# Optimization experiments

Hardware: AMD Instinct MI355X
Metric: run time of the kernel (lower is better)

## Reference

```python
import jax, jax.numpy as jnp
import numpy as np

# ---- fixed configuration (see shape_source) ----
B, ND, NPR = 64, 32, 32          # batch, drug-subgraph nodes, protein-subgraph nodes
LD, LP = 100, 1000               # drug_MAX_LENGH, protein_MAX_LENGH
DIM, CONV = 64, 40               # char_dim, conv
DK, PK = (4, 6, 8), (4, 8, 12)   # drug_kernel, protein_kernel
VD, VP = 71, 26                  # SMILES / FASTA vocab sizes
ED, EP, EDP = 128, 128, 64       # DDI / PPI / DPI edges per subgraph
GNN_LAYERS = 2
SLOPE = 0.01                     # LeakyReLU default slope


def setup_inputs():
    key = jax.random.key(0)
    ks = iter(jax.random.split(key, 64))
    def nrm(shape, s=0.02):
        return jax.random.normal(next(ks), shape, jnp.float32) * s
    inp = {}
    inp['drug_tokens'] = jax.random.randint(next(ks), (B, LD), 0, VD, jnp.int32)
    inp['protein_tokens'] = jax.random.randint(next(ks), (B, LP), 0, VP, jnp.int32)
    inp['drug_node_tokens'] = jax.random.randint(next(ks), (B, ND, LD), 0, VD, jnp.int32)
    inp['protein_node_tokens'] = jax.random.randint(next(ks), (B, NPR, LP), 0, VP, jnp.int32)
    inp['ddi_edges'] = jax.random.randint(next(ks), (B, 2, ED), 0, ND, jnp.int32)
    inp['ppi_edges'] = jax.random.randint(next(ks), (B, 2, EP), 0, NPR, jnp.int32)
    inp['dpi_edges'] = jax.random.randint(next(ks), (B, 2, EDP), 0, min(ND, NPR), jnp.int32)
    # sequence embeddings (padding_idx=0 -> zero row)
    inp['drug_embed'] = nrm((VD, DIM)).at[0].set(0.)
    inp['protein_embed'] = nrm((VP, DIM)).at[0].set(0.)
    # drug CNN stack
    inp['dW1'], inp['db1'] = nrm((CONV, DIM, DK[0])), jnp.zeros((CONV,), jnp.float32)
    inp['dW2'], inp['db2'] = nrm((2*CONV, CONV, DK[1])), jnp.zeros((2*CONV,), jnp.float32)
    inp['dW3'], inp['db3'] = nrm((4*CONV, 2*CONV, DK[2])), jnp.zeros((4*CONV,), jnp.float32)
    # protein CNN stack
    inp['pW1'], inp['pb1'] = nrm((CONV, DIM, PK[0])), jnp.zeros((CONV,), jnp.float32)
    inp['pW2'], inp['pb2'] = nrm((2*CONV, CONV, PK[1])), jnp.zeros((2*CONV,), jnp.float32)
    inp['pW3'], inp['pb3'] = nrm((4*CONV, 2*CONV, PK[2])), jnp.zeros((4*CONV,), jnp.float32)
    # graph node-feature embedding tables (creat_drug_node / creat_protein_node)
    inp['drug_node_table'] = nrm((VD, LD)).at[0].set(0.)
    inp['protein_node_table'] = nrm((VP, LP)).at[0].set(0.)
    # SAGEConv params: Wl (neighbor path, has bias), Wr (root path, no bias)
    inp['ddi_Wl'], inp['ddi_bl'], inp['ddi_Wr'] = nrm((LD, LD)), jnp.zeros((LD,), jnp.float32), nrm((LD, LD))
    inp['ppi_Wl'], inp['ppi_bl'], inp['ppi_Wr'] = nrm((LP, LP)), jnp.zeros((LP,), jnp.float32), nrm((LP, LP))
    inp['dpi_Wl'], inp['dpi_bl'], inp['dpi_Wr'] = nrm((LP, LD)), jnp.zeros((LP,), jnp.float32), nrm((LP, LP))
    inp['pdi_Wl'], inp['pdi_bl'], inp['pdi_Wr'] = nrm((LD, LP)), jnp.zeros((LD,), jnp.float32), nrm((LD, LD))
    # fusion MLP
    inp['fc1_W'], inp['fc1_b'] = nrm((1024, 1420)), jnp.zeros((1024,), jnp.float32)
    inp['fc2_W'], inp['fc2_b'] = nrm((1024, 1024)), jnp.zeros((1024,), jnp.float32)
    inp['fc3_W'], inp['fc3_b'] = nrm((512, 1024)), jnp.zeros((512,), jnp.float32)
    inp['out_W'], inp['out_b'] = nrm((2, 512)), jnp.zeros((2,), jnp.float32)
    return inp


def _conv_relu(x, w, b):
    # x: [B, Cin, L], w: [Cout, Cin, K] -> valid Conv1d + ReLU
    y = jax.lax.conv_general_dilated(x, w, (1,), 'VALID',
                                     dimension_numbers=('NCH', 'OIH', 'NCH'))
    return jax.nn.relu(y + b[None, :, None])


def _node_feat(tokens, table, vocab):
    # mean over sequence of embedded tokens == (token-count histogram / L) @ table
    counts = jax.nn.one_hot(tokens, vocab, dtype=table.dtype).sum(axis=2)  # [B, N, V]
    return jnp.einsum('bnv,vd->bnd', counts, table) / tokens.shape[-1]


def _sage(xs, xd, edges, Wl, bl, Wr):
    # PyG SAGEConv, aggr='mean': lin_l(mean_j x_src[j]) + lin_r(x_dst)
    src, dst = edges[0], edges[1]
    n = xd.shape[0]
    s = jax.ops.segment_sum(xs[src], dst, num_segments=n)
    c = jax.ops.segment_sum(jnp.ones((src.shape[0],), xs.dtype), dst, num_segments=n)
    agg = s / jnp.maximum(c, 1.0)[:, None]
    return agg @ Wl.T + bl + xd @ Wr.T


def _forward(drug_tokens, protein_tokens, drug_node_tokens, protein_node_tokens,
             ddi_edges, ppi_edges, dpi_edges,
             drug_embed, protein_embed,
             dW1, db1, dW2, db2, dW3, db3,
             pW1, pb1, pW2, pb2, pW3, pb3,
             drug_node_table, protein_node_table,
             ddi_Wl, ddi_bl, ddi_Wr, ppi_Wl, ppi_bl, ppi_Wr,
             dpi_Wl, dpi_bl, dpi_Wr, pdi_Wl, pdi_bl, pdi_Wr,
             fc1_W, fc1_b, fc2_W, fc2_b, fc3_W, fc3_b, out_W, out_b):
    # --- CNN branches (maxpool kernel spans whole remaining length == global max) ---
    x = drug_embed[drug_tokens].transpose(0, 2, 1)            # [B, DIM, LD]
    for w, b in ((dW1, db1), (dW2, db2), (dW3, db3)):
        x = _conv_relu(x, w, b)
    drug_feat = x.max(axis=2)                                 # [B, 4*CONV]
    y = protein_embed[protein_tokens].transpose(0, 2, 1)      # [B, DIM, LP]
    for w, b in ((pW1, pb1), (pW2, pb2), (pW3, pb3)):
        y = _conv_relu(y, w, b)
    prot_feat = y.max(axis=2)                                 # [B, 4*CONV]
    # --- graph node features: mean over sequence of node-token embeddings ---
    dx = _node_feat(drug_node_tokens, drug_node_table, VD)    # [B, ND, LD]
    px = _node_feat(protein_node_tokens, protein_node_table, VP)  # [B, NPR, LP]
    # --- hetero SAGE message passing, aggr='mean' across relations ---
    def _hetero(dxi, pxi, ddi, ppi, dpi):
        pdi = dpi[::-1]
        d = 0.5 * (_sage(dxi, dxi, ddi, ddi_Wl, ddi_bl, ddi_Wr)
                   + _sage(pxi, dxi, pdi, pdi_Wl, pdi_bl, pdi_Wr))
        p = 0.5 * (_sage(pxi, pxi, ppi, ppi_Wl, ppi_bl, ppi_Wr)
                   + _sage(dxi, pxi, dpi, dpi_Wl, dpi_bl, dpi_Wr))
        return d, p
    hetero_b = jax.vmap(_hetero)
    for _ in range(GNN_LAYERS):
        dx, px = hetero_b(dx, px, ddi_edges, ppi_edges, dpi_edges)
    # node 0 of each subgraph is the query drug / protein
    graph_feat = jnp.concatenate([dx[:, 0], px[:, 0]], axis=-1)   # [B, LD+LP]
    # --- fusion MLP (dropout = identity at eval) ---
    pair = jnp.concatenate([drug_feat, prot_feat, graph_feat], axis=-1)  # [B, 1420]
    h = jax.nn.leaky_relu(pair @ fc1_W.T + fc1_b, SLOPE)
    h = jax.nn.leaky_relu(h @ fc2_W.T + fc2_b, SLOPE)
    h = jax.nn.leaky_relu(h @ fc3_W.T + fc3_b, SLOPE)
    return h @ out_W.T + out_b                                 # [B, 2]


def reference(drug_tokens, protein_tokens, drug_node_tokens, protein_node_tokens,
              ddi_edges, ppi_edges, dpi_edges,
              drug_embed, protein_embed,
              dW1, db1, dW2, db2, dW3, db3,
              pW1, pb1, pW2, pb2, pW3, pb3,
              drug_node_table, protein_node_table,
              ddi_Wl, ddi_bl, ddi_Wr, ppi_Wl, ppi_bl, ppi_Wr,
              dpi_Wl, dpi_bl, dpi_Wr, pdi_Wl, pdi_bl, pdi_Wr,
              fc1_W, fc1_b, fc2_W, fc2_b, fc3_W, fc3_b, out_W, out_b):
    return _forward(drug_tokens, protein_tokens, drug_node_tokens, protein_node_tokens,
                    ddi_edges, ppi_edges, dpi_edges,
                    drug_embed, protein_embed,
                    dW1, db1, dW2, db2, dW3, db3,
                    pW1, pb1, pW2, pb2, pW3, pb3,
                    drug_node_table, protein_node_table,
                    ddi_Wl, ddi_bl, ddi_Wr, ppi_Wl, ppi_bl, ppi_Wr,
                    dpi_Wl, dpi_bl, dpi_Wr, pdi_Wl, pdi_bl, pdi_Wr,
                    fc1_W, fc1_b, fc2_W, fc2_b, fc3_W, fc3_b, out_W, out_b)
```

## Files before the change

### kernel.cpp

```cpp
#include <hip/hip_runtime.h>
#include <hip/hip_bf16.h>


typedef __attribute__((ext_vector_type(8))) short short8;
typedef __attribute__((ext_vector_type(4))) float f32x4;
union FragU { uint32_t u[4]; uint4 q; short8 s; };

static __device__ inline unsigned short f2bf(float v) {
    __hip_bfloat16 h = __float2bfloat16(v);
    return *(unsigned short*)&h;
}

static constexpr size_t O_PAIR = 0;
static constexpr size_t O_CF1  = 363520;
static constexpr size_t O_CF2  = 625664;
static constexpr size_t O_CF3  = 887808;
static constexpr size_t Z1_END = 1018880;
static constexpr size_t O_H1   = 1018880;
static constexpr size_t O_H2   = 1281024;
static constexpr size_t O_H3   = 1543168;
static constexpr size_t O_BD   = 1674240;
static constexpr size_t O_BP   = 1674752;
static constexpr size_t O_WDS  = 1678848;
static constexpr size_t O_WPS  = 1998336;
static constexpr size_t O_WTP1 = 6520320;
static constexpr size_t O_WTP2 = 6585856;
static constexpr size_t O_WTP3 = 6667776;
static constexpr size_t O_WTD1 = 7159296;
static constexpr size_t O_WTD2 = 7224832;
static constexpr size_t O_WTD3 = 7306752;
static constexpr size_t AR     = 7552512;
static constexpr size_t A_AD  = AR + 0;
static constexpr size_t A_AP  = AR + 479232;
static constexpr size_t A_A2D = AR + 1327104;
static constexpr size_t A_A2P = AR + 1486848;
static constexpr size_t A_UD  = AR + 1769472;
static constexpr size_t A_UP  = AR + 1855488;
static constexpr size_t A_RHO = AR + 2641920;
static constexpr size_t Z2_CNT = 2641920 / 4;
static constexpr size_t A_Y2P = AR + 0;
static constexpr size_t A_Y1P = AR + 10158080;
static constexpr size_t A_Y1D = AR + 15278080;
static constexpr size_t A_Y2D = AR + 10158080;
static constexpr size_t NEED_BYTES = AR + 15810560;

__global__ void zero32_k(uint32_t* __restrict__ p, int n) {
    int i = blockIdx.x * 256 + threadIdx.x;
    if (i < n) p[i] = 0u;
}

__global__ void zero2_k(uint32_t* __restrict__ p1, int n1,
                        uint32_t* __restrict__ p2, int n2) {
    int i = blockIdx.x * 256 + threadIdx.x;
    if (i < n1) p1[i] = 0u;
    else if (i - n1 < n2) p2[i - n1] = 0u;
}

static constexpr long P0 = 100;
static constexpr long P1 = P0 + 1000;
static constexpr long P2 = P1 + 14336;
static constexpr long P3 = P2 + 14336;
static constexpr long P4 = P3 + 131072;
static constexpr long P5 = P4 + 1048576;
static constexpr long P6 = P5 + 1048576;
static constexpr long P7 = P6 + 163840;
static constexpr long P8 = P7 + 131072;
static constexpr long P9 = P8 + 32768;
static constexpr long P10 = P9 + 40960;
static constexpr long P11 = P10 + 245760;
static constexpr long P12 = P11 + 32768;
static constexpr long P13 = P12 + 40960;
static constexpr long P14 = P13 + 122880;
static constexpr long P15 = P14 + 70400;

__device__ inline void wt_block(unsigned short* dst, int ld_dst, int coloff,
                                const float* s1, const float* s2, int ld_src,
                                int N, int Kreal, int Kblk, long local) {
    int n = (int)(local / Kblk), k = (int)(local % Kblk);
    float v = 0.f;
    if (n < N && k < Kreal) {
        v = s1[(size_t)n * ld_src + k];
        if (s2) v += s2[(size_t)n * ld_src + k];
    }
    dst[(size_t)n * ld_dst + coloff + k] = f2bf(v);
}

__device__ inline void wtconv_block(unsigned short* dst, const float* W,
                                    int Co, int Ci, int K, int KP, long local) {
    int co = (int)(local / (Ci * KP));
    int rem = (int)(local % (Ci * KP));
    int ci = rem / KP, k = rem % KP;
    float v = (co < Co && k < K) ? W[((size_t)co * Ci + ci) * K + k] : 0.f;
    dst[local] = f2bf(v);
}

__global__ __launch_bounds__(256) void prep_k(
    float* bd, float* bp, unsigned short* WdS, unsigned short* WpS,
    unsigned short* WtP1, unsigned short* WtP2, unsigned short* WtP3,
    unsigned short* WtD1, unsigned short* WtD2, unsigned short* WtD3,
    float* pair,
    const float* ddi_Wl, const float* ddi_bl, const float* ddi_Wr,
    const float* ppi_Wl, const float* ppi_bl, const float* ppi_Wr,
    const float* dpi_Wl, const float* dpi_bl, const float* dpi_Wr,
    const float* pdi_Wl, const float* pdi_bl, const float* pdi_Wr,
    const float* dW1, const float* dW2, const float* dW3,
    const float* pW1, const float* pW2, const float* pW3) {
    long idx = (long)blockIdx.x * 256 + threadIdx.x;
    if (idx < P0) { bd[idx] = 0.5f * (ddi_bl[idx] + pdi_bl[idx]); return; }
    if (idx < P1) { long j = idx - P0; bp[j] = 0.5f * (ppi_bl[j] + dpi_bl[j]); return; }
    if (idx < P2) { wt_block(WdS, 1248, 0, ddi_Wl, nullptr, 100, 100, 100, 112, idx - P1); return; }
    if (idx < P3) { wt_block(WdS, 1248, 112, ddi_Wr, pdi_Wr, 100, 100, 100, 112, idx - P2); return; }
    if (idx < P4) { wt_block(WdS, 1248, 224, pdi_Wl, nullptr, 1000, 100, 1000, 1024, idx - P3); return; }
    if (idx < P5) { wt_block(WpS, 2208, 0, ppi_Wl, nullptr, 1000, 1000, 1000, 1024, idx - P4); return; }
    if (idx < P6) { wt_block(WpS, 2208, 1024, ppi_Wr, dpi_Wr, 1000, 1000, 1000, 1024, idx - P5); return; }
    if (idx < P7) { wt_block(WpS, 2208, 2048, dpi_Wl, nullptr, 100, 1000, 100, 160, idx - P6); return; }
    if (idx < P8)  { return; }
    if (idx < P9)  { wtconv_block(WtP1, pW1, 40, 64, 4, 8, idx - P8); return; }
    if (idx < P10) { wtconv_block(WtP2, pW2, 80, 40, 8, 8, idx - P9); return; }
    if (idx < P11) { wtconv_block(WtP3, pW3, 160, 80, 12, 16, idx - P10); return; }
    if (idx < P12) { wtconv_block(WtD1, dW1, 40, 64, 4, 8, idx - P11); return; }
    if (idx < P13) { wtconv_block(WtD2, dW2, 80, 40, 6, 8, idx - P12); return; }
    if (idx < P14) { wtconv_block(WtD3, dW3, 160, 80, 8, 8, idx - P13); return; }
    if (idx < P15) {
        long l = idx - P14;
        int b = (int)(l / 1100), j = (int)(l % 1100);
        if (j < 100) pair[(size_t)b * 1420 + 320 + j] = bd[j];
        else pair[(size_t)b * 1420 + 420 + (j - 100)] = bp[j - 100];
        return;
    }
}

__global__ __launch_bounds__(256) void gnn_front_k(const int* __restrict__ ddi,
                                                   const int* __restrict__ ppi,
                                                   const int* __restrict__ dpi,
                                                   const int* __restrict__ dtoks,
                                                   const int* __restrict__ ptoks,
                                                   const float* __restrict__ dtable,
                                                   const float* __restrict__ ptable,
                                                   float* __restrict__ RHO,
                                                   unsigned short* __restrict__ Ad,
                                                   unsigned short* __restrict__ Ap) {
    const int role = blockIdx.x, b = blockIdx.y, tid = threadIdx.x;
    __shared__ float M[4][32][32];
    __shared__ int cnt4[4][32];
// ... 107 lines not shown
                #pragma unroll
                for (int i = 0; i < 7; ++i) acc[i] += WC[i][v] * tv;
            }
            unsigned short h;
            h = f2bf(acc[0]); Ad[g0d + 224 + d] = h;
            h = f2bf(acc[1]); Ad[g1d_ + 224 + d] = h; Ap[g0p + 1024 + d] = h;
            h = f2bf(acc[2]); Ap[g0p + d] = h;
            h = f2bf(acc[3]); Ap[g1p + d] = h;
            h = f2bf(acc[4]); Ap[g1p + 1024 + d] = h; Ap[g2p + d] = h;
            h = f2bf(acc[5]); Ap[g2p + 1024 + d] = h;
            h = f2bf(acc[6]); Ad[g2d + 224 + d] = h;
        }
    }
}

__global__ __launch_bounds__(256) void gemm_sk3(const unsigned short* __restrict__ A, int lda,
                                                const unsigned short* __restrict__ Bm, int ldb,
                                                int K, int KS, float scale,
                                                float* __restrict__ out,
                                                int rs, int coloff, int Nw) {
    const int tid = threadIdx.x;
    const int lane = tid & 63, w = tid >> 6, c = lane & 15, q = lane >> 4;
    const int n = blockIdx.x * 64 + w * 16 + c;
    const int gz = blockIdx.z;
    const unsigned short* Ab = A + (size_t)gz * 64 * lda;
    const int Ks = ((K / KS + 31) / 32) * 32;
    const int k0 = blockIdx.y * Ks;
    const int k1 = min(K, k0 + Ks);
    f32x4 acc[4];
    #pragma unroll
    for (int i = 0; i < 4; ++i) acc[i] = (f32x4){0.f, 0.f, 0.f, 0.f};
    for (int k = k0; k < k1; k += 32) {
        FragU bf;
        bf.q = *(const uint4*)&Bm[(size_t)n * ldb + k + q * 8];
        #pragma unroll
        for (int i = 0; i < 4; ++i) {
            FragU af;
            af.q = *(const uint4*)&Ab[(size_t)(i * 16 + c) * lda + k + q * 8];
            acc[i] = __builtin_amdgcn_mfma_f32_16x16x32_bf16(af.s, bf.s, acc[i], 0, 0, 0);
        }
    }
    if (n >= Nw) return;
    #pragma unroll
    for (int i = 0; i < 4; ++i)
        #pragma unroll
        for (int r = 0; r < 4; ++r) {
            int m = gz * 64 + i * 16 + q * 4 + r;
            atomicAdd(&out[(size_t)m * rs + coloff + n], scale * acc[i][r]);
        }
}

__global__ void ep_k(const float* __restrict__ Ud, const float* __restrict__ Up,
                     const float* __restrict__ RHO,
                     const float* __restrict__ bd, const float* __restrict__ bp,
                     unsigned short* __restrict__ A2d, unsigned short* __restrict__ A2p) {
    int idx = blockIdx.x * 256 + threadIdx.x;
    if (idx < 192 * 112) {
        int m = idx / 112, n = idx % 112;
        if (n >= 100) return;
        int g = m >> 6, b = m & 63;
        float rho = (g == 0) ? RHO[b * 4 + 0] : (g == 1) ? 1.f : RHO[b * 4 + 3];
        unsigned short h = f2bf(Ud[idx] + rho * bd[n]);
        if (g == 0) A2d[(size_t)b * 1248 + n] = h;
        else if (g == 1) A2d[(size_t)b * 1248 + 112 + n] = h;
        else A2p[(size_t)b * 2208 + 2048 + n] = h;
    } else {
        int l = idx - 192 * 112;
        if (l >= 192 * 1024) return;
        int m = l / 1024, n = l % 1024;
        if (n >= 1000) return;
        int g = m >> 6, b = m & 63;
        float rho = (g == 0) ? RHO[b * 4 + 1] : (g == 1) ? RHO[b * 4 + 2] : 1.f;
        unsigned short h = f2bf(Up[l] + rho * bp[n]);
        if (g == 0) A2d[(size_t)b * 1248 + 224 + n] = h;
        else if (g == 1) A2p[(size_t)b * 2208 + n] = h;
        else A2p[(size_t)b * 2208 + 1024 + n] = h;
    }
}

template <int KP>
__device__ __forceinline__ void conv_body(const unsigned short* __restrict__ xin,
                                          int Ci, int Lp,
                                          const unsigned short* __restrict__ Wt, int KK,
                                          int nchunk,
                                          const float* __restrict__ bias, int Co,
                                          unsigned short* __restrict__ yout,
                                          int Lout, int LoutPad,
                                          float* __restrict__ pool, int pool_coloff,
                                          int b, int co0, int t0,
                                          unsigned short* As, unsigned short* xraw) {
    constexpr int CIPC = 64 / KP;
    constexpr int LG = (KP == 8) ? 3 : 4;
    const int tid = threadIdx.x;
    const int lane = tid & 63, w = tid >> 6, c = lane & 15, q = lane >> 4;
    f32x4 acc[4][4];
    #pragma unroll
    for (int i = 0; i < 4; ++i)
        #pragma unroll
        for (int j = 0; j < 4; ++j) acc[i][j] = (f32x4){0.f, 0.f, 0.f, 0.f};
    const int row8 = tid >> 3, col8 = (tid & 7) * 8;
    for (int ch = 0; ch < nchunk; ++ch) {
        const int kkbase = ch * 64, ci0 = ch * CIPC;
        #pragma unroll
        for (int p = 0; p < 2; ++p) {
            int row = row8 + p * 32;
            *(uint4*)&As[row * 72 + col8] =
                *(const uint4*)&Wt[(size_t)(co0 + row) * KK + kkbase + col8];
        }
        for (int gi = tid; gi < CIPC * 34; gi += 256) {
            int ci = gi / 34, g8 = (gi % 34) * 8, gt = t0 + g8;
            const unsigned short* src = xin + ((size_t)b * Ci + ci0 + ci) * Lp + gt;
            if (gt + 8 <= Lp) {
                *(uint4*)&xraw[ci * 272 + g8] = *(const uint4*)src;
            } else {
                #pragma unroll
                for (int jj = 0; jj < 8; ++jj)
                    xraw[ci * 272 + g8 + jj] = (gt + jj < Lp) ? src[jj] : (unsigned short)0;
            }
        }
        __syncthreads();
        #pragma unroll
        for (int ks = 0; ks < 2; ++ks) {
            const int kc = ks * 32;
            FragU af[4];
            #pragma unroll
            for (int i = 0; i < 4; ++i)
                af[i].q = *(const uint4*)&As[(i * 16 + c) * 72 + kc + q * 8];
            const int koff = kc + q * 8;
            const int cioff = koff >> LG;
            const int k0 = koff & (KP - 1);
            const uint32_t* xr = (const uint32_t*)xraw + cioff * 136;
            #pragma unroll
            for (int j = 0; j < 4; ++j) {
                int tt = w * 64 + j * 16 + c;
                int eoff = tt + k0;
                int d0 = eoff >> 1;
                unsigned sh = (unsigned)(eoff & 1) * 16u;
                uint32_t u0 = xr[d0], u1 = xr[d0 + 1], u2 = xr[d0 + 2],
                         u3 = xr[d0 + 3], u4 = xr[d0 + 4];
                FragU bf;
                bf.u[0] = __builtin_amdgcn_alignbit(u1, u0, sh);
                bf.u[1] = __builtin_amdgcn_alignbit(u2, u1, sh);
                bf.u[2] = __builtin_amdgcn_alignbit(u3, u2, sh);
                bf.u[3] = __builtin_amdgcn_alignbit(u4, u3, sh);
                #pragma unroll
                for (int i = 0; i < 4; ++i)
                    acc[i][j] = __builtin_amdgcn_mfma_f32_16x16x32_bf16(af[i].s, bf.s,
                                                                        acc[i][j], 0, 0, 0);
            }
        }
        __syncthreads();
    }
    if (pool) {
        #pragma unroll
        for (int i = 0; i < 4; ++i) {
            #pragma unroll
            for (int r = 0; r < 4; ++r) {
                int co = co0 + i * 16 + q * 4 + r;
                float bv = (co < Co) ? bias[co] : 0.f;
                float v = 0.f;
                #pragma unroll
                for (int j = 0; j < 4; ++j) {
                    int t = t0 + w * 64 + j * 16 + c;
                    if (t < Lout) v = fmaxf(v, fmaxf(acc[i][j][r] + bv, 0.f));
                }
                v = fmaxf(v, __shfl_xor(v, 1));
                v = fmaxf(v, __shfl_xor(v, 2));
                v = fmaxf(v, __shfl_xor(v, 4));
                v = fmaxf(v, __shfl_xor(v, 8));
                if (c == 0 && co < Co)
                    atomicMax((int*)&pool[(size_t)b * 1420 + pool_coloff + co],
                              __float_as_int(v));
            }
        }
    } else {
        #pragma unroll
        for (int i = 0; i < 4; ++i) {
            #pragma unroll
            for (int r = 0; r < 4; ++r) {
                int co = co0 + i * 16 + q * 4 + r;
                if (co >= Co) continue;
                float bv = bias[co];
                #pragma unroll
                for (int j = 0; j < 4; ++j) {
                    int t = t0 + w * 64 + j * 16 + c;
                    if (t < Lout) {
                        yout[((size_t)b * Co + co) * LoutPad + t] =
                            f2bf(fmaxf(acc[i][j][r] + bv, 0.f));
                    } else if (t < LoutPad) {
                        yout[((size_t)b * Co + co) * LoutPad + t] = 0;
                    }
                }
            }
        }
    }
}

template <int KP>
__global__ __launch_bounds__(256) void conv_mfma(const unsigned short* __restrict__ xin,
                                                 int Ci, int Lp,
                                                 const unsigned short* __restrict__ Wt, int KK,
                                                 int nchunk,
                                                 const float* __restrict__ bias, int Co,
                                                 unsigned short* __restrict__ yout,
                                                 int Lout, int LoutPad,
                                                 float* __restrict__ pool, int pool_coloff) {
    __shared__ __align__(16) unsigned short As[64 * 72];
    __shared__ __align__(16) unsigned short xraw[(64 / KP) * 272];
    conv_body<KP>(xin, Ci, Lp, Wt, KK, nchunk, bias, Co, yout, Lout, LoutPad,
                  pool, pool_coloff, blockIdx.z, blockIdx.y * 64, blockIdx.x * 256,
                  As, xraw);
}

__device__ __forceinline__ void conv1e_body(const int* __restrict__ toks,
                                            const float* __restrict__ table, int V, int L,
                                            const unsigned short* __restrict__ Wt, int KK,
                                            const float* __restrict__ bias, int Co,
                                            unsigned short* __restrict__ yout,
                                            int Lout, int LoutPad,
                                            int b, int co0, int t0,
                                            unsigned short* As, unsigned short* xraw,
                                            unsigned short* tabT, int* tok_s) {
    const int tid = threadIdx.x;
    const int lane = tid & 63, w = tid >> 6, c = lane & 15, q = lane >> 4;
    for (int idx = tid; idx < 64 * V; idx += 256) {
        int ci = idx / V, v = idx % V;
        tabT[ci * 72 + v] = f2bf(table[(size_t)v * 64 + ci]);
    }
// ... 18 lines not shown
        }
        for (int gi = tid; gi < 8 * 272; gi += 256) {
            int ci = gi / 272, t = gi % 272;
            xraw[gi] = tabT[(ci0 + ci) * 72 + tok_s[t]];
        }
        __syncthreads();
        #pragma unroll
        for (int ks = 0; ks < 2; ++ks) {
            const int kc = ks * 32;
            FragU af[4];
            #pragma unroll
            for (int i = 0; i < 4; ++i)
                af[i].q = *(const uint4*)&As[(i * 16 + c) * 72 + kc + q * 8];
            const int koff = kc + q * 8;
            const int cioff = koff >> 3;
            const int k0 = koff & 7;
            const uint32_t* xr = (const uint32_t*)xraw + cioff * 136;
            #pragma unroll
            for (int j = 0; j < 4; ++j) {
                int tt = w * 64 + j * 16 + c;
                int eoff = tt + k0;
                int d0 = eoff >> 1;
                unsigned sh = (unsigned)(eoff & 1) * 16u;
                uint32_t u0 = xr[d0], u1 = xr[d0 + 1], u2 = xr[d0 + 2],
                         u3 = xr[d0 + 3], u4 = xr[d0 + 4];
                FragU bf;
                bf.u[0] = __builtin_amdgcn_alignbit(u1, u0, sh);
                bf.u[1] = __builtin_amdgcn_alignbit(u2, u1, sh);
                bf.u[2] = __builtin_amdgcn_alignbit(u3, u2, sh);
                bf.u[3] = __builtin_amdgcn_alignbit(u4, u3, sh);
                #pragma unroll
                for (int i = 0; i < 4; ++i)
                    acc[i][j] = __builtin_amdgcn_mfma_f32_16x16x32_bf16(af[i].s, bf.s,
                                                                        acc[i][j], 0, 0, 0);
            }
        }
        __syncthreads();
    }
// ... 28 lines not shown
    __shared__ __align__(16) unsigned short As[64 * 72];
    __shared__ __align__(16) unsigned short xraw[8 * 272];
    __shared__ unsigned short tabT[64 * 72];
    __shared__ int tok_s[272];
    int z = blockIdx.z;
    if (z < 64) {
        conv1e_body(ptoks, ptable, 26, 1000, WtP1, 512, pb1, 40, y1p, 997, 1000,
                    z, blockIdx.y * 64, blockIdx.x * 256, As, xraw, tabT, tok_s);
    } else {
        if (blockIdx.x > 0) return;
        conv1e_body(dtoks, dtable, 71, 100, WtD1, 512, db1, 40, y1d, 97, 104,
                    z - 64, blockIdx.y * 64, 0, As, xraw, tabT, tok_s);
    }
}

__global__ __launch_bounds__(256) void conv3_dual(
    const unsigned short* __restrict__ y2p, const unsigned short* __restrict__ WtP3,
    const float* __restrict__ pb3, float* __restrict__ pair,
    const unsigned short* __restrict__ y1d, const unsigned short* __restrict__ WtD2,
    const float* __restrict__ db2, unsigned short* __restrict__ y2d) {
    __shared__ __align__(16) unsigned short As[64 * 72];
    __shared__ __align__(16) unsigned short xraw[8 * 272];
    int z = blockIdx.z;
    if (z < 64) {
        conv_body<16>(y2p, 80, 992, WtP3, 1280, 20, pb3, 160, nullptr, 979, 0,
                      pair, 160, z, blockIdx.y * 64, blockIdx.x * 256, As, xraw);
    } else {
        if (blockIdx.x > 0 || blockIdx.y > 1) return;
        conv_body<8>(y1d, 40, 104, WtD2, 320, 5, db2, 80, y2d, 92, 96,
                     nullptr, 0, z - 64, blockIdx.y * 64, 0, As, xraw);
    }
}

__global__ __launch_bounds__(256) void gemm_nt(const float* __restrict__ A, int lda,
                                               const float* __restrict__ Bm,
                                               float* __restrict__ Cout,
                                               int M, int N, int K, int KC) {
    const int m0 = blockIdx.x * 64, n0 = blockIdx.y * 64, s = blockIdx.z;
    const int tid = threadIdx.x, ty = tid >> 4, tx = tid & 15;
    __shared__ __align__(16) float As[16][68];
    __shared__ __align__(16) float Bs[16][68];
    float acc[4][4] = {};
    const int kbeg = s * KC, kend = min(K, kbeg + KC);
    for (int k0 = kbeg; k0 < kend; k0 += 16) {
        int colk = k0 + tx;
        bool kok = colk < kend;
        #pragma unroll
        for (int qq = 0; qq < 4; ++qq) {
            int mi = ty + qq * 16;
            As[tx][mi] = (kok && (m0 + mi) < M) ? A[(size_t)(m0 + mi) * lda + colk] : 0.f;
            Bs[tx][mi] = (kok && (n0 + mi) < N) ? Bm[(size_t)(n0 + mi) * K + colk] : 0.f;
        }
        __syncthreads();
        #pragma unroll
        for (int kk = 0; kk < 16; ++kk) {
            float4 a4 = *(const float4*)&As[kk][ty * 4];
            float4 b4 = *(const float4*)&Bs[kk][tx * 4];
            float av[4] = {a4.x, a4.y, a4.z, a4.w};
            float bv[4] = {b4.x, b4.y, b4.z, b4.w};
            #pragma unroll
            for (int i = 0; i < 4; ++i)
                #pragma unroll
                for (int j = 0; j < 4; ++j)
                    acc[i][j] = fmaf(av[i], bv[j], acc[i][j]);
        }
        __syncthreads();
    }
    #pragma unroll
    for (int i = 0; i < 4; ++i) {
        int m = m0 + ty * 4 + i;
        if (m >= M) continue;
        #pragma unroll
        for (int j = 0; j < 4; ++j) {
            int n = n0 + tx * 4 + j;
            if (n >= N) continue;
            atomicAdd(&Cout[(size_t)m * N + n], acc[i][j]);
        }
    }
}

__global__ void epilogue_k(const float* __restrict__ C, const float* __restrict__ bias,
                           float* __restrict__ out, int M, int N, int act) {
    int idx = blockIdx.x * 256 + threadIdx.x;
    if (idx >= M * N) return;
    int m = idx / N, n = idx % N;
    float v = C[idx] + bias[n];
    if (act == 2) v = v >= 0.f ? v : 0.01f * v;
    out[(size_t)m * N + n] = v;
}

__global__ void out_k(const float* __restrict__ h3, const float* __restrict__ W,
                      const float* __restrict__ bias, float* __restrict__ out) {
    int tid = threadIdx.x;
    if (tid >= 128) return;
    int b = tid >> 1, n = tid & 1;
    const float* hr = h3 + (size_t)b * 512;
    const float* wr = W + (size_t)n * 512;
    float a = 0.f;
    for (int k = 0; k < 512; ++k) a = fmaf(hr[k], wr[k], a);
    out[b * 2 + n] = a + bias[n];
}

static inline int kc_of(int K, int S) { return ((K + S * 16 - 1) / (S * 16)) * 16; }
static inline dim3 g1d(int n) { return dim3((n + 255) / 256); }

extern "C" void kernel_launch(void* const* d_in, const int* in_sizes, int n_in,
                              void* d_out, int out_size, void* d_ws, size_t ws_size,
                              hipStream_t stream) {
    const int* drug_tokens       = (const int*)d_in[0];
    const int* protein_tokens    = (const int*)d_in[1];
    const int* drug_node_tokens  = (const int*)d_in[2];
    const int* protein_node_toks = (const int*)d_in[3];
    const int* ddi_edges         = (const int*)d_in[4];
    const int* ppi_edges         = (const int*)d_in[5];
// ... 18 lines not shown
    const float* pdi_Wr = (const float*)d_in[34];
    const float* fc1_W = (const float*)d_in[35]; const float* fc1_b = (const float*)d_in[36];
    const float* fc2_W = (const float*)d_in[37]; const float* fc2_b = (const float*)d_in[38];
    const float* fc3_W = (const float*)d_in[39]; const float* fc3_b = (const float*)d_in[40];
    const float* out_W = (const float*)d_in[41]; const float* out_b = (const float*)d_in[42];

    float* outp = (float*)d_out;
    if (ws_size < NEED_BYTES) {
        zero32_k<<<g1d(out_size), 256, 0, stream>>>((uint32_t*)outp, out_size);
        return;
    }
    char* wsb = (char*)d_ws;
    float* pair = (float*)(wsb + O_PAIR);
    float* cf1 = (float*)(wsb + O_CF1); float* cf2 = (float*)(wsb + O_CF2);
    float* cf3 = (float*)(wsb + O_CF3);
    float* h1 = (float*)(wsb + O_H1); float* h2 = (float*)(wsb + O_H2);
    float* h3 = (float*)(wsb + O_H3);
    float* bd = (float*)(wsb + O_BD); float* bp = (float*)(wsb + O_BP);
    unsigned short* WdS  = (unsigned short*)(wsb + O_WDS);
    unsigned short* WpS  = (unsigned short*)(wsb + O_WPS);
    unsigned short* WtP1 = (unsigned short*)(wsb + O_WTP1);
    unsigned short* WtP2 = (unsigned short*)(wsb + O_WTP2);
    unsigned short* WtP3 = (unsigned short*)(wsb + O_WTP3);
    unsigned short* WtD1 = (unsigned short*)(wsb + O_WTD1);
    unsigned short* WtD2 = (unsigned short*)(wsb + O_WTD2);
    unsigned short* WtD3 = (unsigned short*)(wsb + O_WTD3);
    unsigned short* Ad  = (unsigned short*)(wsb + A_AD);
    unsigned short* Ap  = (unsigned short*)(wsb + A_AP);
    unsigned short* A2d = (unsigned short*)(wsb + A_A2D);
    unsigned short* A2p = (unsigned short*)(wsb + A_A2P);
    float* Ud  = (float*)(wsb + A_UD);
    float* Up  = (float*)(wsb + A_UP);
    float* RHO = (float*)(wsb + A_RHO);
    unsigned short* y2p = (unsigned short*)(wsb + A_Y2P);
    unsigned short* y1p = (unsigned short*)(wsb + A_Y1P);
    unsigned short* y1d = (unsigned short*)(wsb + A_Y1D);
    unsigned short* y2d = (unsigned short*)(wsb + A_Y2D);

    zero2_k<<<g1d((int)(Z1_END / 4 + Z2_CNT)), 256, 0, stream>>>(
        (uint32_t*)wsb, (int)(Z1_END / 4), (uint32_t*)(wsb + A_AD), (int)Z2_CNT);

    prep_k<<<g1d((int)P15), 256, 0, stream>>>(bd, bp, WdS, WpS,
                                              WtP1, WtP2, WtP3, WtD1, WtD2, WtD3, pair,
                                              ddi_Wl, ddi_bl, ddi_Wr,
                                              ppi_Wl, ppi_bl, ppi_Wr,
                                              dpi_Wl, dpi_bl, dpi_Wr,
                                              pdi_Wl, pdi_bl, pdi_Wr,
                                              dW1, dW2, dW3, pW1, pW2, pW3);

    gnn_front_k<<<dim3(2, 64), 256, 0, stream>>>(ddi_edges, ppi_edges, dpi_edges,
                                                 drug_node_tokens, protein_node_toks,
                                                 drug_node_table, prot_node_table,
                                                 RHO, Ad, Ap);

    gemm_sk3<<<dim3(2, 8, 3), 256, 0, stream>>>(Ad, 1248, WdS, 1248, 1248, 8, 0.5f,
                                                Ud, 112, 0, 100);
    gemm_sk3<<<dim3(16, 8, 3), 256, 0, stream>>>(Ap, 2208, WpS, 2208, 2208, 8, 0.5f,
                                                 Up, 1024, 0, 1000);
    ep_k<<<g1d(192 * 112 + 192 * 1024), 256, 0, stream>>>(Ud, Up, RHO, bd, bp, A2d, A2p);

    gemm_sk3<<<dim3(2, 8, 1), 256, 0, stream>>>(A2d, 1248, WdS, 1248, 1248, 8, 0.5f,
                                                pair, 1420, 320, 100);
    gemm_sk3<<<dim3(16, 8, 1), 256, 0, stream>>>(A2p, 2208, WpS, 2208, 2208, 8, 0.5f,
                                                 pair, 1420, 420, 1000);

    conv1_dual<<<dim3(4, 1, 128), 256, 0, stream>>>(protein_tokens, protein_embed,
                                                    WtP1, pb1, y1p,
                                                    drug_tokens, drug_embed,
                                                    WtD1, db1, y1d);
    conv_mfma<8><<<dim3(4, 2, 64), 256, 0, stream>>>(y1p, 40, 1000, WtP2, 320, 5,
                                                     pb2, 80, y2p, 990, 992, nullptr, 0);
    conv3_dual<<<dim3(4, 3, 128), 256, 0, stream>>>(y2p, WtP3, pb3, pair,
                                                    y1d, WtD2, db2, y2d);
    conv_mfma<8><<<dim3(1, 3, 64), 256, 0, stream>>>(y2d, 80, 96, WtD3, 640, 10,
                                                     db3, 160, nullptr, 85, 0, pair, 0);

    gemm_nt<<<dim3(1, 16, 16), 256, 0, stream>>>(pair, 1420, fc1_W, cf1, 64, 1024, 1420, kc_of(1420, 16));
    epilogue_k<<<g1d(64 * 1024), 256, 0, stream>>>(cf1, fc1_b, h1, 64, 1024, 2);
    gemm_nt<<<dim3(1, 16, 16), 256, 0, stream>>>(h1, 1024, fc2_W, cf2, 64, 1024, 1024, kc_of(1024, 16));
    epilogue_k<<<g1d(64 * 1024), 256, 0, stream>>>(cf2, fc2_b, h2, 64, 1024, 2);
    gemm_nt<<<dim3(1, 8, 16), 256, 0, stream>>>(h2, 1024, fc3_W, cf3, 64, 512, 1024, kc_of(1024, 16));
    epilogue_k<<<g1d(64 * 512), 256, 0, stream>>>(cf3, fc3_b, h3, 64, 512, 2);
    out_k<<<dim3(1), 128, 0, stream>>>(h3, out_W, out_b, outp);
}
```

Before: 517.1 us.

## Merge launches: fold zeroing into prep, fuse split-K and conv stages, inline epilogues

Folds the workspace zeroing kernel into prep_k. Merges the drug and protein split-K GEMMs into one launch per stage, and likewise merges the conv2 and conv3 stages into dual kernels with a wider 128-row output tile. The bias+LeakyReLU epilogue kernels are removed: that work is applied when the next GEMM or out_k loads its A operand. The aim is to cut launch count and the intermediate round-trips through global memory. The cost is extra branch divergence in prep_k, idle blocks in the padded grids, and more registers held by the larger conv tile.

```diff
diff --git a/kernel.cpp b/kernel.cpp
--- a/kernel.cpp
+++ b/kernel.cpp
@@ -15,21 +15,17 @@
 static constexpr size_t O_CF1  = 363520;
 static constexpr size_t O_CF2  = 625664;
 static constexpr size_t O_CF3  = 887808;
-static constexpr size_t Z1_END = 1018880;
-static constexpr size_t O_H1   = 1018880;
-static constexpr size_t O_H2   = 1281024;
-static constexpr size_t O_H3   = 1543168;
-static constexpr size_t O_BD   = 1674240;
-static constexpr size_t O_BP   = 1674752;
-static constexpr size_t O_WDS  = 1678848;
-static constexpr size_t O_WPS  = 1998336;
-static constexpr size_t O_WTP1 = 6520320;
-static constexpr size_t O_WTP2 = 6585856;
-static constexpr size_t O_WTP3 = 6667776;
-static constexpr size_t O_WTD1 = 7159296;
-static constexpr size_t O_WTD2 = 7224832;
-static constexpr size_t O_WTD3 = 7306752;
-static constexpr size_t AR     = 7552512;
+static constexpr size_t O_BD   = 1018880;
+static constexpr size_t O_BP   = 1019392;
+static constexpr size_t O_WDS  = 1023488;
+static constexpr size_t O_WPS  = 1342976;
+static constexpr size_t O_WTP1 = 5864960;
+static constexpr size_t O_WTP2 = 5930496;
+static constexpr size_t O_WTP3 = 6012416;
+static constexpr size_t O_WTD1 = 6503936;
+static constexpr size_t O_WTD2 = 6569472;
+static constexpr size_t O_WTD3 = 6651392;
+static constexpr size_t AR     = 6897152;
 static constexpr size_t A_AD  = AR + 0;
 static constexpr size_t A_AP  = AR + 479232;
 static constexpr size_t A_A2D = AR + 1327104;
@@ -37,41 +33,36 @@
 static constexpr size_t A_UD  = AR + 1769472;
 static constexpr size_t A_UP  = AR + 1855488;
 static constexpr size_t A_RHO = AR + 2641920;
-static constexpr size_t Z2_CNT = 2641920 / 4;
+static constexpr size_t GNN_BYTES = 2642944;
 static constexpr size_t A_Y2P = AR + 0;
 static constexpr size_t A_Y1P = AR + 10158080;
 static constexpr size_t A_Y1D = AR + 15278080;
-static constexpr size_t A_Y2D = AR + 10158080;
-static constexpr size_t NEED_BYTES = AR + 15810560;
+static constexpr size_t A_Y2D = AR + 15810560;
+static constexpr size_t NEED_BYTES = AR + 16793600;
 
 __global__ void zero32_k(uint32_t* __restrict__ p, int n) {
     int i = blockIdx.x * 256 + threadIdx.x;
     if (i < n) p[i] = 0u;
 }
 
-__global__ void zero2_k(uint32_t* __restrict__ p1, int n1,
-                        uint32_t* __restrict__ p2, int n2) {
-    int i = blockIdx.x * 256 + threadIdx.x;
-    if (i < n1) p1[i] = 0u;
-    else if (i - n1 < n2) p2[i - n1] = 0u;
-}
-
-static constexpr long P0 = 100;
-static constexpr long P1 = P0 + 1000;
-static constexpr long P2 = P1 + 14336;
-static constexpr long P3 = P2 + 14336;
-static constexpr long P4 = P3 + 131072;
-static constexpr long P5 = P4 + 1048576;
-static constexpr long P6 = P5 + 1048576;
-static constexpr long P7 = P6 + 163840;
-static constexpr long P8 = P7 + 131072;
-static constexpr long P9 = P8 + 32768;
-static constexpr long P10 = P9 + 40960;
-static constexpr long P11 = P10 + 245760;
-static constexpr long P12 = P11 + 32768;
-static constexpr long P13 = P12 + 40960;
-static constexpr long P14 = P13 + 122880;
-static constexpr long P15 = P14 + 70400;
+static constexpr long Q0 = 100;
+static constexpr long Q1 = Q0 + 1000;
+static constexpr long Q2 = Q1 + 14336;
+static constexpr long Q3 = Q2 + 14336;
+static constexpr long Q4 = Q3 + 131072;
+static constexpr long Q5 = Q4 + 1048576;
+static constexpr long Q6 = Q5 + 1048576;
+static constexpr long Q7 = Q6 + 163840;
+static constexpr long Q8 = Q7 + 32768;
+static constexpr long Q9 = Q8 + 40960;
+static constexpr long Q10 = Q9 + 245760;
+static constexpr long Q11 = Q10 + 32768;
+static constexpr long Q12 = Q11 + 40960;
+static constexpr long Q13 = Q12 + 122880;
+static constexpr long Q14 = Q13 + 70400;
+static constexpr long Q15 = Q14 + 20480;
+static constexpr long Q16 = Q15 + 163840;
+static constexpr long Q17 = Q16 + 660736;
 
 __device__ inline void wt_block(unsigned short* dst, int ld_dst, int coloff,
                                 const float* s1, const float* s2, int ld_src,
@@ -98,7 +89,7 @@
     float* bd, float* bp, unsigned short* WdS, unsigned short* WpS,
     unsigned short* WtP1, unsigned short* WtP2, unsigned short* WtP3,
     unsigned short* WtD1, unsigned short* WtD2, unsigned short* WtD3,
-    float* pair,
+    float* pair, float* cfz, uint32_t* gnnz,
     const float* ddi_Wl, const float* ddi_bl, const float* ddi_Wr,
     const float* ppi_Wl, const float* ppi_bl, const float* ppi_Wr,
     const float* dpi_Wl, const float* dpi_bl, const float* dpi_Wr,
@@ -106,28 +97,35 @@
     const float* dW1, const float* dW2, const float* dW3,
     const float* pW1, const float* pW2, const float* pW3) {
     long idx = (long)blockIdx.x * 256 + threadIdx.x;
-    if (idx < P0) { bd[idx] = 0.5f * (ddi_bl[idx] + pdi_bl[idx]); return; }
-    if (idx < P1) { long j = idx - P0; bp[j] = 0.5f * (ppi_bl[j] + dpi_bl[j]); return; }
-    if (idx < P2) { wt_block(WdS, 1248, 0, ddi_Wl, nullptr, 100, 100, 100, 112, idx - P1); return; }
-    if (idx < P3) { wt_block(WdS, 1248, 112, ddi_Wr, pdi_Wr, 100, 100, 100, 112, idx - P2); return; }
-    if (idx < P4) { wt_block(WdS, 1248, 224, pdi_Wl, nullptr, 1000, 100, 1000, 1024, idx - P3); return; }
-    if (idx < P5) { wt_block(WpS, 2208, 0, ppi_Wl, nullptr, 1000, 1000, 1000, 1024, idx - P4); return; }
-    if (idx < P6) { wt_block(WpS, 2208, 1024, ppi_Wr, dpi_Wr, 1000, 1000, 1000, 1024, idx - P5); return; }
-    if (idx < P7) { wt_block(WpS, 2208, 2048, dpi_Wl, nullptr, 100, 1000, 100, 160, idx - P6); return; }
-    if (idx < P8)  { return; }
-    if (idx < P9)  { wtconv_block(WtP1, pW1, 40, 64, 4, 8, idx - P8); return; }
-    if (idx < P10) { wtconv_block(WtP2, pW2, 80, 40, 8, 8, idx - P9); return; }
-    if (idx < P11) { wtconv_block(WtP3, pW3, 160, 80, 12, 16, idx - P10); return; }
-    if (idx < P12) { wtconv_block(WtD1, dW1, 40, 64, 4, 8, idx - P11); return; }
-    if (idx < P13) { wtconv_block(WtD2, dW2, 80, 40, 6, 8, idx - P12); return; }
-    if (idx < P14) { wtconv_block(WtD3, dW3, 160, 80, 8, 8, idx - P13); return; }
-    if (idx < P15) {
-        long l = idx - P14;
+    if (idx < Q0) { bd[idx] = 0.5f * (ddi_bl[idx] + pdi_bl[idx]); return; }
+    if (idx < Q1) { long j = idx - Q0; bp[j] = 0.5f * (ppi_bl[j] + dpi_bl[j]); return; }
+    if (idx < Q2) { wt_block(WdS, 1248, 0, ddi_Wl, nullptr, 100, 100, 100, 112, idx - Q1); return; }
+    if (idx < Q3) { wt_block(WdS, 1248, 112, ddi_Wr, pdi_Wr, 100, 100, 100, 112, idx - Q2); return; }
+    if (idx < Q4) { wt_block(WdS, 1248, 224, pdi_Wl, nullptr, 1000, 100, 1000, 1024, idx - Q3); return; }
+    if (idx < Q5) { wt_block(WpS, 2208, 0, ppi_Wl, nullptr, 1000, 1000, 1000, 1024, idx - Q4); return; }
+    if (idx < Q6) { wt_block(WpS, 2208, 1024, ppi_Wr, dpi_Wr, 1000, 1000, 1000, 1024, idx - Q5); return; }
+    if (idx < Q7) { wt_block(WpS, 2208, 2048, dpi_Wl, nullptr, 100, 1000, 100, 160, idx - Q6); return; }
+    if (idx < Q8)  { wtconv_block(WtP1, pW1, 40, 64, 4, 8, idx - Q7); return; }
+    if (idx < Q9)  { wtconv_block(WtP2, pW2, 80, 40, 8, 8, idx - Q8); return; }
+    if (idx < Q10) { wtconv_block(WtP3, pW3, 160, 80, 12, 16, idx - Q9); return; }
+    if (idx < Q11) { wtconv_block(WtD1, dW1, 40, 64, 4, 8, idx - Q10); return; }
+    if (idx < Q12) { wtconv_block(WtD2, dW2, 80, 40, 6, 8, idx - Q11); return; }
+    if (idx < Q13) { wtconv_block(WtD3, dW3, 160, 80, 8, 8, idx - Q12); return; }
+    if (idx < Q14) {
+        long l = idx - Q13;
         int b = (int)(l / 1100), j = (int)(l % 1100);
-        if (j < 100) pair[(size_t)b * 1420 + 320 + j] = bd[j];
-        else pair[(size_t)b * 1420 + 420 + (j - 100)] = bp[j - 100];
+        if (j < 100) pair[(size_t)b * 1420 + 320 + j] = 0.5f * (ddi_bl[j] + pdi_bl[j]);
+        else { int j2 = j - 100; pair[(size_t)b * 1420 + 420 + j2] = 0.5f * (ppi_bl[j2] + dpi_bl[j2]); }
         return;
     }
+    if (idx < Q15) {
+        long l = idx - Q14;
+        int b = (int)(l / 320), j = (int)(l % 320);
+        pair[(size_t)b * 1420 + j] = 0.f;
+        return;
+    }
+    if (idx < Q16) { cfz[idx - Q15] = 0.f; return; }
+    if (idx < Q17) { gnnz[idx - Q16] = 0u; return; }
 }
 
 __global__ __launch_bounds__(256) void gnn_front_k(const int* __restrict__ ddi,
@@ -265,18 +263,18 @@
     }
 }
 
-__global__ __launch_bounds__(256) void gemm_sk3(const unsigned short* __restrict__ A, int lda,
-                                                const unsigned short* __restrict__ Bm, int ldb,
-                                                int K, int KS, float scale,
-                                                float* __restrict__ out,
-                                                int rs, int coloff, int Nw) {
+__device__ __forceinline__ void sk_body(const unsigned short* __restrict__ A, int lda,
+                                        const unsigned short* __restrict__ Bm, int ldb,
+                                        int K, int KS, float scale,
+                                        float* __restrict__ out,
+                                        int rs, int coloff, int Nw,
+                                        int bx, int by, int gz) {
     const int tid = threadIdx.x;
     const int lane = tid & 63, w = tid >> 6, c = lane & 15, q = lane >> 4;
-    const int n = blockIdx.x * 64 + w * 16 + c;
-    const int gz = blockIdx.z;
+    const int n = bx * 64 + w * 16 + c;
     const unsigned short* Ab = A + (size_t)gz * 64 * lda;
     const int Ks = ((K / KS + 31) / 32) * 32;
-    const int k0 = blockIdx.y * Ks;
+    const int k0 = by * Ks;
     const int k1 = min(K, k0 + Ks);
     f32x4 acc[4];
     #pragma unroll
@@ -299,6 +297,39 @@
             int m = gz * 64 + i * 16 + q * 4 + r;
             atomicAdd(&out[(size_t)m * rs + coloff + n], scale * acc[i][r]);
         }
+}
+
+__global__ __launch_bounds__(256) void sk_stage1(const unsigned short* __restrict__ Ad,
+                                                 const unsigned short* __restrict__ WdS,
+                                                 float* __restrict__ Ud,
+                                                 const unsigned short* __restrict__ Ap,
+                                                 const unsigned short* __restrict__ WpS,
+                                                 float* __restrict__ Up) {
+    int z = blockIdx.z;
+    if (z < 3) {
+        sk_body(Ap, 2208, WpS, 2208, 2208, 8, 0.5f, Up, 1024, 0, 1000,
+                blockIdx.x, blockIdx.y, z);
+    } else {
+        if (blockIdx.x >= 2) return;
+        sk_body(Ad, 1248, WdS, 1248, 1248, 8, 0.5f, Ud, 112, 0, 100,
+                blockIdx.x, blockIdx.y, z - 3);
+    }
+}
+
+__global__ __launch_bounds__(256) void sk_stage2(const unsigned short* __restrict__ A2d,
+                                                 const unsigned short* __restrict__ WdS,
+                                                 const unsigned short* __restrict__ A2p,
+                                                 const unsigned short* __restrict__ WpS,
+                                                 float* __restrict__ pair) {
+    int z = blockIdx.z;
+    if (z == 0) {
+        sk_body(A2p, 2208, WpS, 2208, 2208, 8, 0.5f, pair, 1420, 420, 1000,
+                blockIdx.x, blockIdx.y, 0);
+    } else {
+        if (blockIdx.x >= 2) return;
+        sk_body(A2d, 1248, WdS, 1248, 1248, 8, 0.5f, pair, 1420, 320, 100,
+                blockIdx.x, blockIdx.y, 0);
+    }
 }
 
 __global__ void ep_k(const float* __restrict__ Ud, const float* __restrict__ Up,
@@ -329,7 +360,7 @@
     }
 }
 
-template <int KP>
+template <int KP, int ITILE>
 __device__ __forceinline__ void conv_body(const unsigned short* __restrict__ xin,
                                           int Ci, int Lp,
                                           const unsigned short* __restrict__ Wt, int KK,
@@ -344,16 +375,16 @@
     constexpr int LG = (KP == 8) ? 3 : 4;
     const int tid = threadIdx.x;
     const int lane = tid & 63, w = tid >> 6, c = lane & 15, q = lane >> 4;
-    f32x4 acc[4][4];
+    f32x4 acc[ITILE][4];
     #pragma unroll
-    for (int i = 0; i < 4; ++i)
+    for (int i = 0; i < ITILE; ++i)
         #pragma unroll
         for (int j = 0; j < 4; ++j) acc[i][j] = (f32x4){0.f, 0.f, 0.f, 0.f};
     const int row8 = tid >> 3, col8 = (tid & 7) * 8;
     for (int ch = 0; ch < nchunk; ++ch) {
         const int kkbase = ch * 64, ci0 = ch * CIPC;
         #pragma unroll
-        for (int p = 0; p < 2; ++p) {
+        for (int p = 0; p < ITILE / 2; ++p) {
             int row = row8 + p * 32;
             *(uint4*)&As[row * 72 + col8] =
                 *(const uint4*)&Wt[(size_t)(co0 + row) * KK + kkbase + col8];
@@ -373,9 +404,9 @@
         #pragma unroll
         for (int ks = 0; ks < 2; ++ks) {
             const int kc = ks * 32;
-            FragU af[4];
+            FragU af[ITILE];
             #pragma unroll
-            for (int i = 0; i < 4; ++i)
+            for (int i = 0; i < ITILE; ++i)
                 af[i].q = *(const uint4*)&As[(i * 16 + c) * 72 + kc + q * 8];
             const int koff = kc + q * 8;
             const int cioff = koff >> LG;
@@ -395,7 +426,7 @@
                 bf.u[2] = __builtin_amdgcn_alignbit(u3, u2, sh);
                 bf.u[3] = __builtin_amdgcn_alignbit(u4, u3, sh);
                 #pragma unroll
-                for (int i = 0; i < 4; ++i)
+                for (int i = 0; i < ITILE; ++i)
                     acc[i][j] = __builtin_amdgcn_mfma_f32_16x16x32_bf16(af[i].s, bf.s,
                                                                         acc[i][j], 0, 0, 0);
             }
@@ -404,7 +435,7 @@
     }
     if (pool) {
         #pragma unroll
-        for (int i = 0; i < 4; ++i) {
+        for (int i = 0; i < ITILE; ++i) {
             #pragma unroll
             for (int r = 0; r < 4; ++r) {
                 int co = co0 + i * 16 + q * 4 + r;
@@ -426,7 +457,7 @@
         }
     } else {
         #pragma unroll
-        for (int i = 0; i < 4; ++i) {
+        for (int i = 0; i < ITILE; ++i) {
             #pragma unroll
             for (int r = 0; r < 4; ++r) {
                 int co = co0 + i * 16 + q * 4 + r;
@@ -447,22 +478,6 @@
     }
 }
 
-template <int KP>
-__global__ __launch_bounds__(256) void conv_mfma(const unsigned short* __restrict__ xin,
-                                                 int Ci, int Lp,
-                                                 const unsigned short* __restrict__ Wt, int KK,
-                                                 int nchunk,
-                                                 const float* __restrict__ bias, int Co,
-                                                 unsigned short* __restrict__ yout,
-                                                 int Lout, int LoutPad,
-                                                 float* __restrict__ pool, int pool_coloff) {
-    __shared__ __align__(16) unsigned short As[64 * 72];
-    __shared__ __align__(16) unsigned short xraw[(64 / KP) * 272];
-    conv_body<KP>(xin, Ci, Lp, Wt, KK, nchunk, bias, Co, yout, Lout, LoutPad,
-                  pool, pool_coloff, blockIdx.z, blockIdx.y * 64, blockIdx.x * 256,
-                  As, xraw);
-}
-
 __device__ __forceinline__ void conv1e_body(const int* __restrict__ toks,
                                             const float* __restrict__ table, int V, int L,
                                             const unsigned short* __restrict__ Wt, int KK,
@@ -511,14 +526,12 @@
                 af[i].q = *(const uint4*)&As[(i * 16 + c) * 72 + kc + q * 8];
             const int koff = kc + q * 8;
             const int cioff = koff >> 3;
-            const int k0 = koff & 7;
             const uint32_t* xr = (const uint32_t*)xraw + cioff * 136;
             #pragma unroll
             for (int j = 0; j < 4; ++j) {
                 int tt = w * 64 + j * 16 + c;
-                int eoff = tt + k0;
-                int d0 = eoff >> 1;
-                unsigned sh = (unsigned)(eoff & 1) * 16u;
+                int d0 = tt >> 1;
+                unsigned sh = (unsigned)(tt & 1) * 16u;
                 uint32_t u0 = xr[d0], u1 = xr[d0 + 1], u2 = xr[d0 + 2],
                          u3 = xr[d0 + 3], u4 = xr[d0 + 4];
                 FragU bf;
@@ -577,25 +590,52 @@
     }
 }
 
+__global__ __launch_bounds__(256) void conv2_dual(
+    const unsigned short* __restrict__ y1p, const unsigned short* __restrict__ WtP2,
+    const float* __restrict__ pb2, unsigned short* __restrict__ y2p,
+    const unsigned short* __restrict__ y1d, const unsigned short* __restrict__ WtD2,
+    const float* __restrict__ db2, unsigned short* __restrict__ y2d) {
+    __shared__ __align__(16) unsigned short As[128 * 72];
+    __shared__ __align__(16) unsigned short xraw[8 * 272];
+    int z = blockIdx.z;
+    if (z < 64) {
+        conv_body<8, 8>(y1p, 40, 1000, WtP2, 320, 5, pb2, 80, y2p, 990, 992,
+                        nullptr, 0, z, 0, blockIdx.x * 256, As, xraw);
+    } else {
+        if (blockIdx.x > 0) return;
+        conv_body<8, 8>(y1d, 40, 104, WtD2, 320, 5, db2, 80, y2d, 92, 96,
+                        nullptr, 0, z - 64, 0, 0, As, xraw);
+    }
+}
+
 __global__ __launch_bounds__(256) void conv3_dual(
     const unsigned short* __restrict__ y2p, const unsigned short* __restrict__ WtP3,
     const float* __restrict__ pb3, float* __restrict__ pair,
-    const unsigned short* __restrict__ y1d, const unsigned short* __restrict__ WtD2,
-    const float* __restrict__ db2, unsigned short* __restrict__ y2d) {
-    __shared__ __align__(16) unsigned short As[64 * 72];
+    const unsigned short* __restrict__ y2d, const unsigned short* __restrict__ WtD3,
+    const float* __restrict__ db3) {
+    __shared__ __align__(16) unsigned short As[128 * 72];
     __shared__ __align__(16) unsigned short xraw[8 * 272];
     int z = blockIdx.z;
     if (z < 64) {
-        conv_body<16>(y2p, 80, 992, WtP3, 1280, 20, pb3, 160, nullptr, 979, 0,
-                      pair, 160, z, blockIdx.y * 64, blockIdx.x * 256, As, xraw);
+        if (blockIdx.y == 0)
+            conv_body<16, 8>(y2p, 80, 992, WtP3, 1280, 20, pb3, 160, nullptr, 979, 0,
+                             pair, 160, z, 0, blockIdx.x * 256, As, xraw);
+        else
+            conv_body<16, 4>(y2p, 80, 992, WtP3, 1280, 20, pb3, 160, nullptr, 979, 0,
+                             pair, 160, z, 128, blockIdx.x * 256, As, xraw);
     } else {
-        if (blockIdx.x > 0 || blockIdx.y > 1) return;
-        conv_body<8>(y1d, 40, 104, WtD2, 320, 5, db2, 80, y2d, 92, 96,
-                     nullptr, 0, z - 64, blockIdx.y * 64, 0, As, xraw);
+        if (blockIdx.x > 0) return;
+        if (blockIdx.y == 0)
+            conv_body<8, 8>(y2d, 80, 96, WtD3, 640, 10, db3, 160, nullptr, 85, 0,
+                            pair, 0, z - 64, 0, 0, As, xraw);
+        else
+            conv_body<8, 4>(y2d, 80, 96, WtD3, 640, 10, db3, 160, nullptr, 85, 0,
+                            pair, 0, z - 64, 128, 0, As, xraw);
     }
 }
 
 __global__ __launch_bounds__(256) void gemm_nt(const float* __restrict__ A, int lda,
+                                               const float* __restrict__ Aep_b,
                                                const float* __restrict__ Bm,
                                                float* __restrict__ Cout,
                                                int M, int N, int K, int KC) {
@@ -611,7 +651,15 @@
         #pragma unroll
         for (int qq = 0; qq < 4; ++qq) {
             int mi = ty + qq * 16;
-            As[tx][mi] = (kok && (m0 + mi) < M) ? A[(size_t)(m0 + mi) * lda + colk] : 0.f;
+            float va = 0.f;
+            if (kok && (m0 + mi) < M) {
+                va = A[(size_t)(m0 + mi) * lda + colk];
+                if (Aep_b) {
+                    va += Aep_b[colk];
+                    va = va >= 0.f ? va : 0.01f * va;
+                }
+            }
+            As[tx][mi] = va;
             Bs[tx][mi] = (kok && (n0 + mi) < N) ? Bm[(size_t)(n0 + mi) * K + colk] : 0.f;
         }
         __syncthreads();
@@ -642,25 +690,19 @@
     }
 }
 
-__global__ void epilogue_k(const float* __restrict__ C, const float* __restrict__ bias,
-                           float* __restrict__ out, int M, int N, int act) {
-    int idx = blockIdx.x * 256 + threadIdx.x;
-    if (idx >= M * N) return;
-    int m = idx / N, n = idx % N;
-    float v = C[idx] + bias[n];
-    if (act == 2) v = v >= 0.f ? v : 0.01f * v;
-    out[(size_t)m * N + n] = v;
-}
-
-__global__ void out_k(const float* __restrict__ h3, const float* __restrict__ W,
-                      const float* __restrict__ bias, float* __restrict__ out) {
+__global__ void out_k(const float* __restrict__ cf3, const float* __restrict__ b3,
+                      const float* __restrict__ W, const float* __restrict__ bias,
+                      float* __restrict__ out) {
     int tid = threadIdx.x;
     if (tid >= 128) return;
     int b = tid >> 1, n = tid & 1;
-    const float* hr = h3 + (size_t)b * 512;
-    const float* wr = W + (size_t)n * 512;
-    float a = 0.f;
-    for (int k = 0; k < 512; ++k) a = fmaf(hr[k], wr[k], a);
+    const float* hr = cf3 + (size_t)b * 512;
+    const float* wr = W + (size_t)n * 512;    float a = 0.f;
+    for (int k = 0; k < 512; ++k) {
+        float v = hr[k] + b3[k];
+        v = v >= 0.f ? v : 0.01f * v;
+        a = fmaf(v, wr[k], a);
+    }
     out[b * 2 + n] = a + bias[n];
 }
 
@@ -709,8 +751,6 @@
     float* pair = (float*)(wsb + O_PAIR);
     float* cf1 = (float*)(wsb + O_CF1); float* cf2 = (float*)(wsb + O_CF2);
     float* cf3 = (float*)(wsb + O_CF3);
-    float* h1 = (float*)(wsb + O_H1); float* h2 = (float*)(wsb + O_H2);
-    float* h3 = (float*)(wsb + O_H3);
     float* bd = (float*)(wsb + O_BD); float* bp = (float*)(wsb + O_BP);
     unsigned short* WdS  = (unsigned short*)(wsb + O_WDS);
     unsigned short* WpS  = (unsigned short*)(wsb + O_WPS);
@@ -732,11 +772,9 @@
     unsigned short* y1d = (unsigned short*)(wsb + A_Y1D);
     unsigned short* y2d = (unsigned short*)(wsb + A_Y2D);
 
-    zero2_k<<<g1d((int)(Z1_END / 4 + Z2_CNT)), 256, 0, stream>>>(
-        (uint32_t*)wsb, (int)(Z1_END / 4), (uint32_t*)(wsb + A_AD), (int)Z2_CNT);
-
-    prep_k<<<g1d((int)P15), 256, 0, stream>>>(bd, bp, WdS, WpS,
-                                              WtP1, WtP2, WtP3, WtD1, WtD2, WtD3, pair,
+    prep_k<<<g1d((int)Q17), 256, 0, stream>>>(bd, bp, WdS, WpS,
+                                              WtP1, WtP2, WtP3, WtD1, WtD2, WtD3,
+                                              pair, cf1, (uint32_t*)(wsb + A_AD),
                                               ddi_Wl, ddi_bl, ddi_Wr,
                                               ppi_Wl, ppi_bl, ppi_Wr,
                                               dpi_Wl, dpi_bl, dpi_Wr,
@@ -748,33 +786,24 @@
                                                  drug_node_table, prot_node_table,
                                                  RHO, Ad, Ap);
 
-    gemm_sk3<<<dim3(2, 8, 3), 256, 0, stream>>>(Ad, 1248, WdS, 1248, 1248, 8, 0.5f,
-                                                Ud, 112, 0, 100);
-    gemm_sk3<<<dim3(16, 8, 3), 256, 0, stream>>>(Ap, 2208, WpS, 2208, 2208, 8, 0.5f,
-                                                 Up, 1024, 0, 1000);
+    sk_stage1<<<dim3(16, 8, 6), 256, 0, stream>>>(Ad, WdS, Ud, Ap, WpS, Up);
     ep_k<<<g1d(192 * 112 + 192 * 1024), 256, 0, stream>>>(Ud, Up, RHO, bd, bp, A2d, A2p);
-
-    gemm_sk3<<<dim3(2, 8, 1), 256, 0, stream>>>(A2d, 1248, WdS, 1248, 1248, 8, 0.5f,
-                                                pair, 1420, 320, 100);
-    gemm_sk3<<<dim3(16, 8, 1), 256, 0, stream>>>(A2p, 2208, WpS, 2208, 2208, 8, 0.5f,
-                                                 pair, 1420, 420, 1000);
+    sk_stage2<<<dim3(16, 8, 2), 256, 0, stream>>>(A2d, WdS, A2p, WpS, pair);
 
     conv1_dual<<<dim3(4, 1, 128), 256, 0, stream>>>(protein_tokens, protein_embed,
                                                     WtP1, pb1, y1p,
                                                     drug_tokens, drug_embed,
                                                     WtD1, db1, y1d);
-    conv_mfma<8><<<dim3(4, 2, 64), 256, 0, stream>>>(y1p, 40, 1000, WtP2, 320, 5,
-                                                     pb2, 80, y2p, 990, 992, nullptr, 0);
-    conv3_dual<<<dim3(4, 3, 128), 256, 0, stream>>>(y2p, WtP3, pb3, pair,
+    conv2_dual<<<dim3(4, 1, 128), 256, 0, stream>>>(y1p, WtP2, pb2, y2p,
                                                     y1d, WtD2, db2, y2d);
-    conv_mfma<8><<<dim3(1, 3, 64), 256, 0, stream>>>(y2d, 80, 96, WtD3, 640, 10,
-                                                     db3, 160, nullptr, 85, 0, pair, 0);
-
-    gemm_nt<<<dim3(1, 16, 16), 256, 0, stream>>>(pair, 1420, fc1_W, cf1, 64, 1024, 1420, kc_of(1420, 16));
-    epilogue_k<<<g1d(64 * 1024), 256, 0, stream>>>(cf1, fc1_b, h1, 64, 1024, 2);
-    gemm_nt<<<dim3(1, 16, 16), 256, 0, stream>>>(h1, 1024, fc2_W, cf2, 64, 1024, 1024, kc_of(1024, 16));
-    epilogue_k<<<g1d(64 * 1024), 256, 0, stream>>>(cf2, fc2_b, h2, 64, 1024, 2);
-    gemm_nt<<<dim3(1, 8, 16), 256, 0, stream>>>(h2, 1024, fc3_W, cf3, 64, 512, 1024, kc_of(1024, 16));
-    epilogue_k<<<g1d(64 * 512), 256, 0, stream>>>(cf3, fc3_b, h3, 64, 512, 2);
-    out_k<<<dim3(1), 128, 0, stream>>>(h3, out_W, out_b, outp);
-}
+    conv3_dual<<<dim3(4, 2, 128), 256, 0, stream>>>(y2p, WtP3, pb3, pair,
+                                                    y2d, WtD3, db3);
+
+    gemm_nt<<<dim3(1, 16, 16), 256, 0, stream>>>(pair, 1420, nullptr, fc1_W, cf1,
+                                                 64, 1024, 1420, kc_of(1420, 16));
+    gemm_nt<<<dim3(1, 16, 16), 256, 0, stream>>>(cf1, 1024, fc1_b, fc2_W, cf2,
+                                                 64, 1024, 1024, kc_of(1024, 16));
+    gemm_nt<<<dim3(1, 8, 16), 256, 0, stream>>>(cf2, 1024, fc2_b, fc3_W, cf3,
+                                                64, 512, 1024, kc_of(1024, 16));
+    out_k<<<dim3(1), 128, 0, stream>>>(cf3, fc3_b, out_W, out_b, outp);
+}
```

New measurement: 614.0 us. +18.7%, slower.
